# Kernel optimization log

Hardware: AMD Instinct MI355X
Metric: run time of the kernel (lower is better)

The kernel has to match this reference:

```python
import jax, jax.numpy as jnp
import numpy as np
import math

NEG = -1e9


def maximum_path(neg_cent, text_len, spec_len):
    # neg_cent: [B, Ts, Tt]; monotonic alignment (Viterbi) DP as in VITS.
    B, Ts, Tt = neg_cent.shape
    jj = jnp.arange(Tt)
    tt = jnp.arange(Ts)
    node_mask = (jj[None, None, :] < text_len[:, None, None]) & (tt[None, :, None] < spec_len[:, None, None])
    nc = jnp.where(node_mask, neg_cent, NEG)

    def fstep(q, nc_t):
        # q: [B, Tt] best score ending at text index j at previous frame
        q_shift = jnp.concatenate([jnp.full((B, 1), NEG, q.dtype), q[:, :-1]], axis=1)
        d = q_shift >= q  # True -> came from j-1 (diagonal move)
        q_new = nc_t + jnp.maximum(q, q_shift)
        return q_new, d

    q0 = jnp.broadcast_to(jnp.where(jj == 0, 0.0, NEG), (B, Tt)).astype(neg_cent.dtype)
    _, dirs = jax.lax.scan(fstep, q0, jnp.swapaxes(nc, 0, 1))  # dirs: [Ts, B, Tt]

    def bstep(j, inp):
        t, d_t = inp
        start = (t == spec_len - 1)
        j_eff = jnp.where(start, text_len - 1, j)
        valid = t < spec_len
        emit = ((jj[None, :] == j_eff[:, None]) & valid[:, None]).astype(neg_cent.dtype)
        came_diag = jnp.take_along_axis(d_t, j_eff[:, None], axis=1)[:, 0]
        j_next = jnp.where(valid, jnp.maximum(j_eff - came_diag.astype(j_eff.dtype), 0), j_eff)
        return j_next, emit

    j_init = jnp.zeros((B,), text_len.dtype)
    _, path = jax.lax.scan(bstep, j_init, (jnp.arange(Ts), dirs), reverse=True)
    return jnp.swapaxes(path, 0, 1)  # [B, Ts, Tt]


def setup_inputs() -> dict:
    B, C, Ts, Tt = 16, 192, 2048, 512
    key = jax.random.key(0)
    k1, k2, k3, k4, k5 = jax.random.split(key, 5)
    z_p = jax.random.normal(k1, (B, C, Ts), dtype=jnp.float32)
    m_p = jax.random.normal(k2, (B, C, Tt), dtype=jnp.float32)
    logs_p = 0.1 * jax.random.normal(k3, (B, C, Tt), dtype=jnp.float32)
    text_len = jax.random.randint(k4, (B,), Tt // 2, Tt + 1, dtype=jnp.int32)
    extra = jax.random.randint(k5, (B,), 0, Ts - Tt + 1, dtype=jnp.int32)
    spec_len = jnp.minimum(text_len + extra, Ts)
    return {"z_p": z_p, "m_p": m_p, "logs_p": logs_p, "spec_len": spec_len, "text_len": text_len}


def reference(z_p, m_p, logs_p, spec_len, text_len):
    B, C, Ts = z_p.shape
    Tt = m_p.shape[2]
    text_mask = (jnp.arange(Tt)[None, :] < text_len[:, None]).astype(z_p.dtype)[:, None, :]  # [B,1,Tt]
    spec_mask = (jnp.arange(Ts)[None, :] < spec_len[:, None]).astype(z_p.dtype)[:, None, :]  # [B,1,Ts]

    # --- neg_cent (torch.no_grad block) ---
    s_p_sq_r = jnp.exp(-2.0 * logs_p)  # [B,C,Tt]
    neg_cent1 = jnp.sum(-0.5 * math.log(2.0 * math.pi) - logs_p, axis=1, keepdims=True)  # [B,1,Tt]
    neg_cent2 = jnp.einsum('bct,bcu->btu', -0.5 * z_p ** 2, s_p_sq_r)  # [B,Ts,Tt]
    neg_cent3 = jnp.einsum('bct,bcu->btu', z_p, m_p * s_p_sq_r)  # [B,Ts,Tt]
    neg_cent4 = jnp.sum(-0.5 * m_p ** 2 * s_p_sq_r, axis=1, keepdims=True)  # [B,1,Tt]
    neg_cent = neg_cent1 + neg_cent2 + neg_cent3 + neg_cent4

    path = jax.lax.stop_gradient(maximum_path(neg_cent, text_len, spec_len))  # [B,Ts,Tt]

    duration = jnp.sum(path, axis=1)[:, None, :]  # [B,1,Tt]
    logw_ = jnp.log(duration + 1e-6) * text_mask  # [B,1,Tt]

    # expand prior stats along the alignment path: [B,C,Ts]
    m_p_exp = jnp.einsum('btu,bcu->bct', path, m_p)
    logs_p_exp = jnp.einsum('btu,bcu->bct', path, logs_p)

    return (path, duration, logw_, m_p_exp, logs_p_exp, text_mask, spec_mask)
```

## Files before the change

kernel.cpp:

```cpp
#include <hip/hip_runtime.h>
#include <hip/hip_bf16.h>
#include <math.h>

#define BB 16
#define CC 192
#define TS 2048
#define TT 512
#define KK 384

#define OFF_PATH 0
#define OFF_DUR  (16777216)
#define OFF_LOGW (OFF_DUR + 8192)
#define OFF_MEXP (OFF_LOGW + 8192)
#define OFF_LEXP (OFF_MEXP + 6291456)
#define OFF_TMASK (OFF_LEXP + 6291456)
#define OFF_SMASK (OFF_TMASK + 8192)

#define NEGC  (-1e9)
#define NEGCF (-1e9f)

__global__ __launch_bounds__(512) void vits_prep(
    const float* __restrict__ m_p, const float* __restrict__ logs_p,
    const int* __restrict__ spec_len, const int* __restrict__ text_len,
    float* __restrict__ Bmat, float* __restrict__ avec,
    float* __restrict__ tmask, float* __restrict__ smask)
{
    const int b = blockIdx.x;
    const int u = threadIdx.x;
    const float C0 = -0.91893853320467274178f;
    float a_acc = 0.f;
    for (int c = 0; c < CC; ++c) {
        float lg = logs_p[((size_t)b*CC + c)*TT + u];
        float mm = m_p[((size_t)b*CC + c)*TT + u];
        float s  = expf(-2.f*lg);
        float ms = mm * s;
        Bmat[((size_t)b*KK + 2*c    )*TT + u] = ms;
        Bmat[((size_t)b*KK + 2*c + 1)*TT + u] = s;
        a_acc += C0 - lg - 0.5f*mm*ms;
    }
    avec[b*TT + u] = a_acc;
    tmask[b*TT + u] = (u < text_len[b]) ? 1.f : 0.f;
    for (int t = u; t < TS; t += TT)
        smask[b*TS + t] = (t < spec_len[b]) ? 1.f : 0.f;
}

__global__ __launch_bounds__(256) void vits_gemm(
    const float* __restrict__ z, const float* __restrict__ Bmat,
    const float* __restrict__ avec, float* __restrict__ out)
{
    const int b  = blockIdx.z;
    const int t0 = blockIdx.y * 64;
    const int u0 = blockIdx.x * 64;
    __shared__ float As[16][68];
    __shared__ float Bs[16][68];
    const int tid = threadIdx.x;
    const int tx = tid & 15, ty = tid >> 4;
    float acc[4][4] = {};
    const float* zb = z    + (size_t)b * CC * TS;
    const float* Bb = Bmat + (size_t)b * KK * TT;
    for (int kc = 0; kc < KK/16; ++kc) {
        {
            int c_l = tid >> 5;
            int t_l = (tid & 31) * 2;
            const float* zp = zb + (size_t)(kc*8 + c_l)*TS + t0 + t_l;
            float2 zv = *(const float2*)zp;
            float2 z1 = make_float2(zv.x, zv.y);
            float2 z2 = make_float2(-0.5f*zv.x*zv.x, -0.5f*zv.y*zv.y);
            *(float2*)&As[2*c_l  ][t_l] = z1;
            *(float2*)&As[2*c_l+1][t_l] = z2;
            int k_l = tid >> 4;
            int u_l = (tid & 15) * 4;
            const float* bp = Bb + (size_t)(kc*16 + k_l)*TT + u0 + u_l;
            *(float4*)&Bs[k_l][u_l] = *(const float4*)bp;
        }
        __syncthreads();
        #pragma unroll
        for (int kk = 0; kk < 16; ++kk) {
            float4 av = *(const float4*)&As[kk][ty*4];
            float4 bv = *(const float4*)&Bs[kk][tx*4];
            float aa[4] = {av.x, av.y, av.z, av.w};
            float bb[4] = {bv.x, bv.y, bv.z, bv.w};
            #pragma unroll
            for (int i = 0; i < 4; ++i)
                #pragma unroll
                for (int jj = 0; jj < 4; ++jj)
                    acc[i][jj] += aa[i]*bb[jj];
        }
        __syncthreads();
    }
    float4 a4 = *(const float4*)(avec + b*TT + u0 + tx*4);
    float ab[4] = {a4.x, a4.y, a4.z, a4.w};
    #pragma unroll
    for (int i = 0; i < 4; ++i) {
        float4 o;
        o.x = acc[i][0] + ab[0];
        o.y = acc[i][1] + ab[1];
        o.z = acc[i][2] + ab[2];
        o.w = acc[i][3] + ab[3];
        *(float4*)(out + ((size_t)b*TS + t0 + ty*4 + i)*TT + u0 + tx*4) = o;
    }
}

__device__ __forceinline__ float dpp_ror1_f32(float v) {
    union { float f; int i; } u, r;
    u.f = v;
    r.i = __builtin_amdgcn_update_dpp(0, u.i, 0x13C, 0xF, 0xF, false);
    return r.f;
}

#define DIRS(j,w) dirs[((j)<<6) | ((w) ^ ((j) & 31))]
#define RING 8

__global__ __launch_bounds__(512, 1) void vits_dp(
    const float* __restrict__ nc,
    const int* __restrict__ spec_len, const int* __restrict__ text_len,
    float* __restrict__ dur, float* __restrict__ logw, int* __restrict__ jt)
{
    __shared__ unsigned int dirs[TT*(TS/32)];
    __shared__ float qrow[TT];
    __shared__ int Tr[TT + 1];

    const int tid  = threadIdx.x;
    const int lane = tid & 63;
    const int wid  = tid >> 6;
    const int b = blockIdx.x;
    const int SL = spec_len[b], TL = text_len[b];
    const bool w0 = (wid == 0);
    const bool l63 = (lane == 63);

    float qa = (tid == 0)  ? 0.0f : NEGCF;
    float qg = (tid == 64) ? 0.0f : NEGCF;
    unsigned int bits = 0;

    const float* nca = nc + (size_t)b*TS*TT + tid;
    const float* ncg = nca - (w0 ? 0 : 64);

    float pfA[RING], pfG[RING];
    #pragma unroll
    for (int i = 0; i < RING; ++i) {
        int tp = (i < SL) ? i : (SL - 1);
        pfA[i] = nca[(size_t)tp*TT];
        pfG[i] = ncg[(size_t)tp*TT];
    }

    int tb = 0;
    for (; tb + 32 <= SL; tb += 32) {
        #pragma unroll
        for (int s = 0; s < 32; ++s) {
            const int t = tb + s;
            float fa = pfA[s & (RING-1)], fg = pfG[s & (RING-1)];
            int tp = t + RING; if (tp > SL - 1) tp = SL - 1;
            pfA[s & (RING-1)] = nca[(size_t)tp*TT];
            pfG[s & (RING-1)] = ncg[(size_t)tp*TT];

            float x = l63 ? qg : qa;
            float qprev = dpp_ror1_f32(x);
            float rotg  = dpp_ror1_f32(qg);
            bool d = (qprev >= qa);
            bits = (bits << 1) | (unsigned)d;
            qa = fa + fmaxf(qprev, qa);
            float qgn = fg + fmaxf(rotg, qg);
            qg = w0 ? NEGCF : qgn;

            if (s == 31) {
                int w = t >> 5;
                DIRS(tid, w) = bits; bits = 0;
                qrow[tid] = qa;
                __syncthreads();
                if (!w0) qg = qrow[tid - 64];
                __syncthreads();
            }
        }
    }
    for (int t = tb; t < SL; ++t) {
        float fa = nca[(size_t)t*TT];
        float fg = ncg[(size_t)t*TT];
        float x = l63 ? qg : qa;
        float qprev = dpp_ror1_f32(x);
        float rotg  = dpp_ror1_f32(qg);
        bool d = (qprev >= qa);
        bits = (bits << 1) | (unsigned)d;
        qa = fa + fmaxf(qprev, qa);
        float qgn = fg + fmaxf(rotg, qg);
        qg = w0 ? NEGCF : qgn;
    }
    if (SL & 31) {
        int w = SL >> 5, r = SL & 31;
        DIRS(tid, w) = bits << (32 - r);
    }
    __syncthreads();

    for (int i = tid; i <= TT; i += 512) Tr[i] = 0;
    __syncthreads();

    if (tid == 0) {
        Tr[TL] = SL;
        int j = TL - 1, tc = SL - 1;
        while (j > 0 && tc >= 0) {
            int w = tc >> 5;
            int bcur = 31 - (tc & 31);
            unsigned int W = DIRS(j, w) & (0xFFFFFFFFu << bcur);
            if (W) {
                int bp = __ffs(W) - 1;
                int tp = (w << 5) + 31 - bp;
                Tr[j] = tp;
                --j;
                tc = tp - 1;
            } else {
                if (w == 0) break;
                tc = (w << 5) - 1;
            }
        }
    }
    __syncthreads();

    for (int u = tid; u < TT; u += 512) {
        float dv = (u < TL) ? (float)(Tr[u+1] - Tr[u]) : 0.0f;
        dur[b*TT + u] = dv;
        logw[b*TT + u] = (u < TL) ? logf(dv + 1e-6f) : 0.0f;
    }
    for (int u = 0; u < TL; ++u) {
        int t1 = Tr[u+1];
        for (int t = Tr[u] + tid; t < t1; t += 512) jt[b*TS + t] = u;
    }
    for (int t = SL + tid; t < TS; t += 512) jt[b*TS + t] = -1;
}

__global__ void vits_path(const int* __restrict__ jt, float4* __restrict__ path)
{
    int idx = blockIdx.x*blockDim.x + threadIdx.x;
    const int total = BB*TS*(TT/4);
    for (; idx < total; idx += gridDim.x*blockDim.x) {
        int u4 = idx & (TT/4 - 1);
        int bt = idx >> 7;
        int j = jt[bt];
        float4 v = make_float4(0.f,0.f,0.f,0.f);
        int r = j - (u4 << 2);
        if (r >= 0 && r < 4) ((float*)&v)[r] = 1.f;
        path[idx] = v;
    }
}

__global__ void vits_mlexp(const int* __restrict__ jt,
    const float* __restrict__ m_p, const float* __restrict__ logs_p,
    float4* __restrict__ mexp, float4* __restrict__ lexp)
{
    int idx = blockIdx.x*blockDim.x + threadIdx.x;
    const int total = BB*CC*(TS/4);
    for (; idx < total; idx += gridDim.x*blockDim.x) {
        int t4 = idx & (TS/4 - 1);
        int bc = idx >> 9;
        int b = bc / CC;
        int4 jv = *(const int4*)(jt + b*TS + (t4 << 2));
        const float* mrow = m_p    + (size_t)bc*TT;
        const float* lrow = logs_p + (size_t)bc*TT;
        float4 mv, lv;
        mv.x = (jv.x >= 0) ? mrow[jv.x] : 0.f;  lv.x = (jv.x >= 0) ? lrow[jv.x] : 0.f;
        mv.y = (jv.y >= 0) ? mrow[jv.y] : 0.f;  lv.y = (jv.y >= 0) ? lrow[jv.y] : 0.f;
        mv.z = (jv.z >= 0) ? mrow[jv.z] : 0.f;  lv.z = (jv.z >= 0) ? lrow[jv.z] : 0.f;
        mv.w = (jv.w >= 0) ? mrow[jv.w] : 0.f;  lv.w = (jv.w >= 0) ? lrow[jv.w] : 0.f;
        mexp[idx] = mv;
        lexp[idx] = lv;
    }
}

extern "C" void kernel_launch(void* const* d_in, const int* in_sizes, int n_in,
                              void* d_out, int out_size, void* d_ws, size_t ws_size,
                              hipStream_t stream) {
    const float* z_p      = (const float*)d_in[0];
    const float* m_p      = (const float*)d_in[1];
    const float* logs_p   = (const float*)d_in[2];
    const int*   spec_len = (const int*)d_in[3];
    const int*   text_len = (const int*)d_in[4];
    float* out = (float*)d_out;

    float* Bmat = (float*)d_ws;
    float* avec = Bmat + (size_t)BB*KK*TT;
    int*   jt   = (int*)(avec + BB*TT);

    float* path  = out + OFF_PATH;
    float* dur   = out + OFF_DUR;
    float* logw  = out + OFF_LOGW;
    float* mexp  = out + OFF_MEXP;
    float* lexp  = out + OFF_LEXP;
    float* tmask = out + OFF_TMASK;
    float* smask = out + OFF_SMASK;

    vits_prep<<<BB, 512, 0, stream>>>(m_p, logs_p, spec_len, text_len,
                                      Bmat, avec, tmask, smask);
    vits_gemm<<<dim3(TT/64, TS/64, BB), 256, 0, stream>>>(z_p, Bmat, avec, path);
    vits_dp<<<BB, 512, 0, stream>>>(path, spec_len, text_len, dur, logw, jt);
    vits_path<<<2048, 256, 0, stream>>>(jt, (float4*)path);
    vits_mlexp<<<2048, 256, 0, stream>>>(jt, m_p, logs_p, (float4*)mexp, (float4*)lexp);
}
```

Baseline: 482.4 us.

## Split DP columns across 1024 threads with 32-wide ghost halo per wave

The Viterbi DP kernel now launches 1024 threads per batch, so each thread carries one column instead of two. Each wave owns 32 authoritative columns and redundantly recomputes the previous wave's 32 columns as a halo, which is enough to cover one 32-step block between syncs. This shortens the per-step serial work (one DPP rotate and max chain instead of two) and deepens the prefetch ring to 16 rows with the end clamp removed. In exchange it doubles the waves taking part in each barrier, and prefetches can read rows past spec_len, up to 16 rows beyond the batch's slice.

New measurement: 480.3 us. No clear change (-0.4%).

```diff
diff --git a/kernel.cpp b/kernel.cpp
--- a/kernel.cpp
+++ b/kernel.cpp
@@ -16,7 +16,6 @@
 #define OFF_TMASK (OFF_LEXP + 6291456)
 #define OFF_SMASK (OFF_TMASK + 8192)
 
-#define NEGC  (-1e9)
 #define NEGCF (-1e9f)
 
 __global__ __launch_bounds__(512) void vits_prep(
@@ -109,9 +108,9 @@
 }
 
 #define DIRS(j,w) dirs[((j)<<6) | ((w) ^ ((j) & 31))]
-#define RING 8
-
-__global__ __launch_bounds__(512, 1) void vits_dp(
+#define RING 16
+
+__global__ __launch_bounds__(1024, 1) void vits_dp(
     const float* __restrict__ nc,
     const int* __restrict__ spec_len, const int* __restrict__ text_len,
     float* __restrict__ dur, float* __restrict__ logw, int* __restrict__ jt)
@@ -125,72 +124,64 @@
     const int wid  = tid >> 6;
     const int b = blockIdx.x;
     const int SL = spec_len[b], TL = text_len[b];
-    const bool w0 = (wid == 0);
-    const bool l63 = (lane == 63);
-
-    float qa = (tid == 0)  ? 0.0f : NEGCF;
-    float qg = (tid == 64) ? 0.0f : NEGCF;
+    const int col = (wid << 5) + lane - 32;
+    const bool auth = (lane >= 32);
+    const bool w0g  = (wid == 0) && (lane < 32);
+
+    float q = (col == 0) ? 0.0f : NEGCF;
     unsigned int bits = 0;
 
-    const float* nca = nc + (size_t)b*TS*TT + tid;
-    const float* ncg = nca - (w0 ? 0 : 64);
-
-    float pfA[RING], pfG[RING];
+    const int colL = (col < 0) ? 0 : col;
+    const float* ncb = nc + (size_t)b*TS*TT + colL;
+
+    float pf[RING];
     #pragma unroll
-    for (int i = 0; i < RING; ++i) {
-        int tp = (i < SL) ? i : (SL - 1);
-        pfA[i] = nca[(size_t)tp*TT];
-        pfG[i] = ncg[(size_t)tp*TT];
-    }
+    for (int i = 0; i < RING; ++i) pf[i] = ncb[(size_t)i*TT];
+    const float* pcur = ncb + (size_t)RING*TT;
 
     int tb = 0;
     for (; tb + 32 <= SL; tb += 32) {
         #pragma unroll
         for (int s = 0; s < 32; ++s) {
             const int t = tb + s;
-            float fa = pfA[s & (RING-1)], fg = pfG[s & (RING-1)];
-            int tp = t + RING; if (tp > SL - 1) tp = SL - 1;
-            pfA[s & (RING-1)] = nca[(size_t)tp*TT];
-            pfG[s & (RING-1)] = ncg[(size_t)tp*TT];
-
-            float x = l63 ? qg : qa;
-            float qprev = dpp_ror1_f32(x);
-            float rotg  = dpp_ror1_f32(qg);
-            bool d = (qprev >= qa);
+            float f = pf[s & (RING-1)];
+            pf[s & (RING-1)] = *pcur;
+            pcur += TT;
+
+            float qp = dpp_ror1_f32(q);
+            bool d = (qp >= q);
             bits = (bits << 1) | (unsigned)d;
-            qa = fa + fmaxf(qprev, qa);
-            float qgn = fg + fmaxf(rotg, qg);
-            qg = w0 ? NEGCF : qgn;
+            float qn = f + fmaxf(qp, q);
+            q = w0g ? NEGCF : qn;
 
             if (s == 31) {
                 int w = t >> 5;
-                DIRS(tid, w) = bits; bits = 0;
-                qrow[tid] = qa;
+                if (auth) {
+                    DIRS(col, w) = bits;
+                    qrow[col] = q;
+                }
+                bits = 0;
                 __syncthreads();
-                if (!w0) qg = qrow[tid - 64];
+                if (!auth && wid != 0) q = qrow[col];
                 __syncthreads();
             }
         }
     }
     for (int t = tb; t < SL; ++t) {
-        float fa = nca[(size_t)t*TT];
-        float fg = ncg[(size_t)t*TT];
-        float x = l63 ? qg : qa;
-        float qprev = dpp_ror1_f32(x);
-        float rotg  = dpp_ror1_f32(qg);
-        bool d = (qprev >= qa);
+        float f = ncb[(size_t)t*TT];
+        float qp = dpp_ror1_f32(q);
+        bool d = (qp >= q);
         bits = (bits << 1) | (unsigned)d;
-        qa = fa + fmaxf(qprev, qa);
-        float qgn = fg + fmaxf(rotg, qg);
-        qg = w0 ? NEGCF : qgn;
+        float qn = f + fmaxf(qp, q);
+        q = w0g ? NEGCF : qn;
     }
     if (SL & 31) {
         int w = SL >> 5, r = SL & 31;
-        DIRS(tid, w) = bits << (32 - r);
+        if (auth) DIRS(col, w) = bits << (32 - r);
     }
     __syncthreads();
 
-    for (int i = tid; i <= TT; i += 512) Tr[i] = 0;
+    for (int i = tid; i <= TT; i += 1024) Tr[i] = 0;
     __syncthreads();
 
     if (tid == 0) {
@@ -214,16 +205,16 @@
     }
     __syncthreads();
 
-    for (int u = tid; u < TT; u += 512) {
+    for (int u = tid; u < TT; u += 1024) {
         float dv = (u < TL) ? (float)(Tr[u+1] - Tr[u]) : 0.0f;
         dur[b*TT + u] = dv;
         logw[b*TT + u] = (u < TL) ? logf(dv + 1e-6f) : 0.0f;
     }
     for (int u = 0; u < TL; ++u) {
         int t1 = Tr[u+1];
-        for (int t = Tr[u] + tid; t < t1; t += 512) jt[b*TS + t] = u;
-    }
-    for (int t = SL + tid; t < TS; t += 512) jt[b*TS + t] = -1;
+        for (int t = Tr[u] + tid; t < t1; t += 1024) jt[b*TS + t] = u;
+    }
+    for (int t = SL + tid; t < TS; t += 1024) jt[b*TS + t] = -1;
 }
 
 __global__ void vits_path(const int* __restrict__ jt, float4* __restrict__ path)
@@ -289,7 +280,7 @@
     vits_prep<<<BB, 512, 0, stream>>>(m_p, logs_p, spec_len, text_len,
                                       Bmat, avec, tmask, smask);
     vits_gemm<<<dim3(TT/64, TS/64, BB), 256, 0, stream>>>(z_p, Bmat, avec, path);
-    vits_dp<<<BB, 512, 0, stream>>>(path, spec_len, text_len, dur, logw, jt);
+    vits_dp<<<BB, 1024, 0, stream>>>(path, spec_len, text_len, dur, logw, jt);
     vits_path<<<2048, 256, 0, stream>>>(jt, (float4*)path);
     vits_mlexp<<<2048, 256, 0, stream>>>(jt, m_p, logs_p, (float4*)mexp, (float4*)lexp);
 }
```
